# Kernel tuning notes

Hardware: AMD Instinct MI355X
Metric: run time of the kernel (lower is better)

Reference implementation:

```python
import jax, jax.numpy as jnp
import numpy as np

B, T, C, HS = 64, 256, 2048, 128


def setup_inputs() -> dict:
    key = jax.random.key(0)
    k1, k2, k3, k4 = jax.random.split(key, 4)
    x = jax.random.normal(k1, (B, T, C), dtype=jnp.float32)
    # Dense(head_size, use_bias=False) kernels, scaled like glorot-ish init
    Wk = jax.random.normal(k2, (C, HS), dtype=jnp.float32) * (C ** -0.5)
    Wq = jax.random.normal(k3, (C, HS), dtype=jnp.float32) * (C ** -0.5)
    Wv = jax.random.normal(k4, (C, HS), dtype=jnp.float32) * (C ** -0.5)
    return {"x": x, "Wk": Wk, "Wq": Wq, "Wv": Wv}


def reference(x, Wk, Wq, Wv):
    Bn, Tn, Cn = x.shape
    k = jnp.einsum("btc,ch->bth", x, Wk)
    q = jnp.einsum("btc,ch->bth", x, Wq)
    v = jnp.einsum("btc,ch->bth", x, Wv)
    # faithful to source: scores = k @ q^T, scaled by C**-0.5 (input dim!)
    scores = jnp.einsum("bth,bsh->bts", k, q) * (Cn ** -0.5)
    causal = jnp.tril(jnp.ones((Tn, Tn), dtype=bool))  # [T, T]
    scores = jnp.where(causal, scores, -jnp.inf)
    weights = jax.nn.softmax(scores, axis=-1)
    return jnp.einsum("bts,bsh->bth", weights, v)
```

## Files before the change

### kernel.cpp

```cpp
#include <hip/hip_runtime.h>
#include <hip/hip_bf16.h>
#include <cstdint>
#include <cstddef>

#define B_  64
#define T_  256
#define C_  2048
#define HS_ 128
#define N_  384

typedef __bf16 bf16x8 __attribute__((ext_vector_type(8)));
typedef float  floatx4 __attribute__((ext_vector_type(4)));

__device__ __forceinline__ unsigned short f2bf_rne(float f) {
  union { float f; unsigned int u; } v; v.f = f;
  unsigned int r = v.u + 0x7fffu + ((v.u >> 16) & 1u);
  return (unsigned short)(r >> 16);
}
__device__ __forceinline__ unsigned short f2bf(float f) {
  union { float f; unsigned int u; } v; v.f = f;
  return (unsigned short)((v.u + 0x8000u) >> 16);
}

__device__ __forceinline__ void async_copy16(const void* g, void* l) {
  __builtin_amdgcn_global_load_lds(
      (const __attribute__((address_space(1))) unsigned int*)g,
      (__attribute__((address_space(3))) unsigned int*)l, 16, 0, 0);
}

__global__ __launch_bounds__(256) void wt_kernel(
    const float* __restrict__ Wk, const float* __restrict__ Wq,
    const float* __restrict__ Wv, unsigned short* __restrict__ Wt) {
  __shared__ float tile[32][33];
  const int w  = blockIdx.z;
  const int c0 = blockIdx.x * 32;
  const int h0 = blockIdx.y * 32;
  const float* W = (w == 0) ? Wk : (w == 1) ? Wq : Wv;
  const int tx = threadIdx.x & 31, ty = threadIdx.x >> 5;
#pragma unroll
  for (int i = 0; i < 32; i += 8)
    tile[ty + i][tx] = W[(size_t)(c0 + ty + i) * HS_ + h0 + tx];
  __syncthreads();
#pragma unroll
  for (int i = 0; i < 32; i += 8) {
    int hh = ty + i, cc = tx;
    Wt[(size_t)(w * HS_ + h0 + hh) * C_ + c0 + cc] = f2bf_rne(tile[cc][hh]);
  }
}

__global__ __launch_bounds__(256) void qkv_gemm(
    const float* __restrict__ X, const unsigned short* __restrict__ Wt,
    unsigned short* __restrict__ kqv, unsigned short* __restrict__ vT) {
  __shared__ unsigned short As[64 * 72];
  __shared__ unsigned short Bs[128 * 64];

  const int tid  = threadIdx.x;
  const int wave = tid >> 6, lane = tid & 63;
  const int quad = lane >> 4, l16 = lane & 15;

  const int g  = blockIdx.x;
  const int ml = g & 7, q8 = g >> 3;
  const int nb = q8 % 3, mh = q8 / 3;
  const int m0 = (mh * 8 + ml) * 64;
  const int n0 = nb * 128;
  const int wm = (wave >> 1) * 32;
  const int wn = (wave & 1) * 64;

  const int arow = tid >> 4;
  const int achk = tid & 15;

  floatx4 acc[2][4] = {};

  for (int k0 = 0; k0 < C_; k0 += 64) {
#pragma unroll
    for (int r = 0; r < 4; ++r) {
      int slot = (r * 4 + wave) * 64 + lane;
      int n = slot >> 3, sl = slot & 7;
      int c = sl ^ (n & 7);
      async_copy16(Wt + (size_t)(n0 + n) * C_ + k0 + c * 8,
                   &Bs[(size_t)((r * 4 + wave) * 64) * 8]);
    }
    float4 av[4];
#pragma unroll
    for (int r = 0; r < 4; ++r)
      av[r] = *(const float4*)(X + (size_t)(m0 + arow + r * 16) * C_ + k0 + achk * 4);
#pragma unroll
    for (int r = 0; r < 4; ++r) {
      ushort4 b4;
      b4.x = f2bf(av[r].x); b4.y = f2bf(av[r].y);
      b4.z = f2bf(av[r].z); b4.w = f2bf(av[r].w);
      *(ushort4*)&As[(arow + r * 16) * 72 + achk * 4] = b4;
    }
    __syncthreads();

#pragma unroll
    for (int ks = 0; ks < 2; ++ks) {
      bf16x8 af[2], bfv[4];
#pragma unroll
      for (int mt = 0; mt < 2; ++mt)
        af[mt] = *(const bf16x8*)&As[(wm + mt * 16 + l16) * 72 + ks * 32 + quad * 8];
#pragma unroll
      for (int nt = 0; nt < 4; ++nt) {
        int n = wn + nt * 16 + l16;
        int c = ks * 4 + quad;
        bfv[nt] = *(const bf16x8*)&Bs[n * 64 + (c ^ (n & 7)) * 8];
      }
#pragma unroll
      for (int mt = 0; mt < 2; ++mt)
#pragma unroll
        for (int nt = 0; nt < 4; ++nt)
          acc[mt][nt] = __builtin_amdgcn_mfma_f32_16x16x32_bf16(
              af[mt], bfv[nt], acc[mt][nt], 0, 0, 0);
    }
    __syncthreads();
  }

#pragma unroll
  for (int mt = 0; mt < 2; ++mt)
#pragma unroll
    for (int nt = 0; nt < 4; ++nt)
#pragma unroll
      for (int r = 0; r < 4; ++r) {
        int row = m0 + wm + mt * 16 + quad * 4 + r;
        int col = wn + nt * 16 + l16;
        unsigned short us = f2bf(acc[mt][nt][r]);
        kqv[(size_t)row * N_ + n0 + col] = us;
        if (n0 == 256) {
          int bb = row >> 8, tt = row & 255;
          vT[(size_t)bb * HS_ * T_ + (size_t)col * T_ + tt] = us;
        }
      }
}

__global__ __launch_bounds__(64) void attn_kernel(
    const unsigned short* __restrict__ kqv, const unsigned short* __restrict__ vT,
    float* __restrict__ out) {
  __shared__ unsigned short P[16 * 264];
  const int lane = threadIdx.x;
  const int quad = lane >> 4, l16 = lane & 15;
  const int tb = blockIdx.x;
  const int b  = blockIdx.y;
  const int t0 = tb * 16;
  const float scale = 0.022097086912079612f;
  const unsigned short* kq = kqv + (size_t)b * T_ * N_;

  bf16x8 kf[4];
#pragma unroll
  for (int ks = 0; ks < 4; ++ks)
    kf[ks] = *(const bf16x8*)&kq[(size_t)(t0 + l16) * N_ + ks * 32 + quad * 8];

  floatx4 S[16];
#pragma unroll
  for (int st = 0; st < 16; ++st) {
    if (st <= tb) {
      floatx4 a = {};
#pragma unroll
      for (int ks = 0; ks < 4; ++ks) {
        bf16x8 qf = *(const bf16x8*)&kq[(size_t)(st * 16 + l16) * N_ + HS_ +
                                        ks * 32 + quad * 8];
        a = __builtin_amdgcn_mfma_f32_16x16x32_bf16(kf[ks], qf, a, 0, 0, 0);
      }
      S[st] = a;
    }
  }

  float rsum[4] = {0.f, 0.f, 0.f, 0.f};
#pragma unroll
  for (int st = 0; st < 16; ++st) {
    if (st <= tb) {
      int scol = st * 16 + l16;
#pragma unroll
      for (int r = 0; r < 4; ++r) {
        int trow = t0 + quad * 4 + r;
        float p = (scol <= trow) ? __expf(S[st][r] * scale) : 0.f;
        S[st][r] = p;
        rsum[r] += p;
      }
    }
  }
#pragma unroll
  for (int m = 1; m < 16; m <<= 1)
#pragma unroll
    for (int r = 0; r < 4; ++r)
      rsum[r] += __shfl_xor(rsum[r], m, 64);

  const int st_hi = (tb + 2) & ~1;
#pragma unroll
  for (int st = 0; st < 16; ++st) {
    if (st < st_hi) {
#pragma unroll
      for (int r = 0; r < 4; ++r) {
        float p = (st <= tb) ? S[st][r] : 0.f;
        P[(quad * 4 + r) * 264 + st * 16 + l16] = f2bf(p);
      }
    }
  }
  __syncthreads();

  floatx4 oacc[8] = {};
  const unsigned short* vb = vT + (size_t)b * HS_ * T_;
  const int nks = (tb + 2) >> 1;
#pragma unroll
  for (int ks = 0; ks < 8; ++ks) {
    if (ks < nks) {
      bf16x8 pa = *(const bf16x8*)&P[l16 * 264 + ks * 32 + quad * 8];
#pragma unroll
      for (int nt = 0; nt < 8; ++nt) {
        bf16x8 bv = *(const bf16x8*)&vb[(size_t)(nt * 16 + l16) * T_ +
                                        ks * 32 + quad * 8];
        oacc[nt] = __builtin_amdgcn_mfma_f32_16x16x32_bf16(pa, bv, oacc[nt], 0, 0, 0);
      }
    }
  }

  float* ob = out + ((size_t)b * T_ + t0) * HS_;
#pragma unroll
  for (int nt = 0; nt < 8; ++nt)
#pragma unroll
    for (int r = 0; r < 4; ++r) {
      int row = quad * 4 + r;
      ob[(size_t)row * HS_ + nt * 16 + l16] = oacc[nt][r] / rsum[r];
    }
}

extern "C" void kernel_launch(void* const* d_in, const int* in_sizes, int n_in,
                              void* d_out, int out_size, void* d_ws, size_t ws_size,
                              hipStream_t stream) {
  const float* x  = (const float*)d_in[0];
  const float* Wk = (const float*)d_in[1];
  const float* Wq = (const float*)d_in[2];
  const float* Wv = (const float*)d_in[3];
  float* out = (float*)d_out;

  char* ws = (char*)d_ws;
  unsigned short* Wt  = (unsigned short*)(ws);
  unsigned short* kqv = (unsigned short*)(ws + 1572864);
  unsigned short* vT  = (unsigned short*)(ws + 1572864 + 12582912);

  hipLaunchKernelGGL(wt_kernel, dim3(64, 4, 3), dim3(256), 0, stream, Wk, Wq, Wv, Wt);
  hipLaunchKernelGGL(qkv_gemm, dim3(768), dim3(256), 0, stream, x, Wt, kqv, vT);
  hipLaunchKernelGGL(attn_kernel, dim3(16, 64), dim3(64), 0, stream, kqv, vT, out);
}
```

Measured before the change: 254.0 us.

## Restructure QKV GEMM to register-streamed B and split attention across four waves

The QKV GEMM drops the LDS-staged weight tile. Each wave now streams its 48 weight columns straight from global memory into registers, prefetching one k-step ahead, while a double-buffered 64x32 tile of X is converted to bf16 and shared through LDS. The grid becomes 256x2 blocks with launch_bounds(256,2). The attention kernel uses four waves per block that split the score tiles round-robin and the output head dimension in quarters, with per-wave row sums combined through shared memory. The goal is more parallelism and less per-wave serial work, at the cost of the weights no longer being reused through LDS and a k-step of only 32 with a barrier on every iteration.

```diff
diff --git a/kernel.cpp b/kernel.cpp
--- a/kernel.cpp
+++ b/kernel.cpp
@@ -20,12 +20,6 @@
 __device__ __forceinline__ unsigned short f2bf(float f) {
   union { float f; unsigned int u; } v; v.f = f;
   return (unsigned short)((v.u + 0x8000u) >> 16);
-}
-
-__device__ __forceinline__ void async_copy16(const void* g, void* l) {
-  __builtin_amdgcn_global_load_lds(
-      (const __attribute__((address_space(1))) unsigned int*)g,
-      (__attribute__((address_space(3))) unsigned int*)l, 16, 0, 0);
 }
 
 __global__ __launch_bounds__(256) void wt_kernel(
@@ -48,99 +42,103 @@
   }
 }
 
-__global__ __launch_bounds__(256) void qkv_gemm(
+__global__ __launch_bounds__(256, 2) void qkv_gemm(
     const float* __restrict__ X, const unsigned short* __restrict__ Wt,
     unsigned short* __restrict__ kqv, unsigned short* __restrict__ vT) {
-  __shared__ unsigned short As[64 * 72];
-  __shared__ unsigned short Bs[128 * 64];
+  __shared__ unsigned short As[2][64 * 32];
 
   const int tid  = threadIdx.x;
   const int wave = tid >> 6, lane = tid & 63;
   const int quad = lane >> 4, l16 = lane & 15;
 
-  const int g  = blockIdx.x;
-  const int ml = g & 7, q8 = g >> 3;
-  const int nb = q8 % 3, mh = q8 / 3;
-  const int m0 = (mh * 8 + ml) * 64;
-  const int n0 = nb * 128;
-  const int wm = (wave >> 1) * 32;
-  const int wn = (wave & 1) * 64;
-
-  const int arow = tid >> 4;
-  const int achk = tid & 15;
-
-  floatx4 acc[2][4] = {};
-
-  for (int k0 = 0; k0 < C_; k0 += 64) {
-#pragma unroll
-    for (int r = 0; r < 4; ++r) {
-      int slot = (r * 4 + wave) * 64 + lane;
-      int n = slot >> 3, sl = slot & 7;
-      int c = sl ^ (n & 7);
-      async_copy16(Wt + (size_t)(n0 + n) * C_ + k0 + c * 8,
-                   &Bs[(size_t)((r * 4 + wave) * 64) * 8]);
-    }
-    float4 av[4];
-#pragma unroll
-    for (int r = 0; r < 4; ++r)
-      av[r] = *(const float4*)(X + (size_t)(m0 + arow + r * 16) * C_ + k0 + achk * 4);
-#pragma unroll
-    for (int r = 0; r < 4; ++r) {
-      ushort4 b4;
-      b4.x = f2bf(av[r].x); b4.y = f2bf(av[r].y);
-      b4.z = f2bf(av[r].z); b4.w = f2bf(av[r].w);
-      *(ushort4*)&As[(arow + r * 16) * 72 + achk * 4] = b4;
-    }
+  const int m0    = blockIdx.x * 64;
+  const int nbase = blockIdx.y * 192 + wave * 48;
+
+  const int arow  = tid >> 3;
+  const int acol4 = (tid & 7) * 4;
+
+  const float* Xr0 = X + (size_t)(m0 + arow) * C_ + acol4;
+  const float* Xr1 = X + (size_t)(m0 + arow + 32) * C_ + acol4;
+
+  const unsigned short* Bp[3];
+#pragma unroll
+  for (int nt = 0; nt < 3; ++nt)
+    Bp[nt] = Wt + (size_t)(nbase + nt * 16 + l16) * C_ + quad * 8;
+
+  float4 a0 = *(const float4*)(Xr0);
+  float4 a1 = *(const float4*)(Xr1);
+  bf16x8 bcur[3];
+#pragma unroll
+  for (int nt = 0; nt < 3; ++nt) bcur[nt] = *(const bf16x8*)(Bp[nt]);
+
+  floatx4 acc[4][3] = {};
+
+  for (int k = 0; k < 64; ++k) {
+    const int cur = k & 1;
+    ushort4 u0, u1;
+    u0.x = f2bf(a0.x); u0.y = f2bf(a0.y); u0.z = f2bf(a0.z); u0.w = f2bf(a0.w);
+    u1.x = f2bf(a1.x); u1.y = f2bf(a1.y); u1.z = f2bf(a1.z); u1.w = f2bf(a1.w);
+    *(ushort4*)&As[cur][arow * 32 + acol4]        = u0;
+    *(ushort4*)&As[cur][(arow + 32) * 32 + acol4] = u1;
     __syncthreads();
 
-#pragma unroll
-    for (int ks = 0; ks < 2; ++ks) {
-      bf16x8 af[2], bfv[4];
-#pragma unroll
-      for (int mt = 0; mt < 2; ++mt)
-        af[mt] = *(const bf16x8*)&As[(wm + mt * 16 + l16) * 72 + ks * 32 + quad * 8];
-#pragma unroll
-      for (int nt = 0; nt < 4; ++nt) {
-        int n = wn + nt * 16 + l16;
-        int c = ks * 4 + quad;
-        bfv[nt] = *(const bf16x8*)&Bs[n * 64 + (c ^ (n & 7)) * 8];
-      }
-#pragma unroll
-      for (int mt = 0; mt < 2; ++mt)
-#pragma unroll
-        for (int nt = 0; nt < 4; ++nt)
-          acc[mt][nt] = __builtin_amdgcn_mfma_f32_16x16x32_bf16(
-              af[mt], bfv[nt], acc[mt][nt], 0, 0, 0);
-    }
-    __syncthreads();
-  }
-
-#pragma unroll
-  for (int mt = 0; mt < 2; ++mt)
-#pragma unroll
-    for (int nt = 0; nt < 4; ++nt)
+    bf16x8 bnxt[3] = {bcur[0], bcur[1], bcur[2]};
+    if (k < 63) {
+      const int kn = (k + 1) * 32;
+      a0 = *(const float4*)(Xr0 + kn);
+      a1 = *(const float4*)(Xr1 + kn);
+#pragma unroll
+      for (int nt = 0; nt < 3; ++nt)
+        bnxt[nt] = *(const bf16x8*)(Bp[nt] + kn);
+    }
+
+    bf16x8 af[4];
+#pragma unroll
+    for (int mt = 0; mt < 4; ++mt)
+      af[mt] = *(const bf16x8*)&As[cur][(mt * 16 + l16) * 32 + quad * 8];
+#pragma unroll
+    for (int mt = 0; mt < 4; ++mt)
+#pragma unroll
+      for (int nt = 0; nt < 3; ++nt)
+        acc[mt][nt] = __builtin_amdgcn_mfma_f32_16x16x32_bf16(
+            af[mt], bcur[nt], acc[mt][nt], 0, 0, 0);
+#pragma unroll
+    for (int nt = 0; nt < 3; ++nt) bcur[nt] = bnxt[nt];
+  }
+
+#pragma unroll
+  for (int mt = 0; mt < 4; ++mt)
+#pragma unroll
+    for (int nt = 0; nt < 3; ++nt) {
+      const int n = nbase + nt * 16 + l16;
+      const bool isv = (nbase + nt * 16) >= 256;
 #pragma unroll
       for (int r = 0; r < 4; ++r) {
-        int row = m0 + wm + mt * 16 + quad * 4 + r;
-        int col = wn + nt * 16 + l16;
+        int m = m0 + mt * 16 + quad * 4 + r;
         unsigned short us = f2bf(acc[mt][nt][r]);
-        kqv[(size_t)row * N_ + n0 + col] = us;
-        if (n0 == 256) {
-          int bb = row >> 8, tt = row & 255;
-          vT[(size_t)bb * HS_ * T_ + (size_t)col * T_ + tt] = us;
+        kqv[(size_t)m * N_ + n] = us;
+        if (isv) {
+          int bb = m >> 8, tt = m & 255;
+          vT[(size_t)bb * HS_ * T_ + (size_t)(n - 256) * T_ + tt] = us;
         }
       }
-}
-
-__global__ __launch_bounds__(64) void attn_kernel(
+    }
+}
+
+__global__ __launch_bounds__(256) void attn_kernel(
     const unsigned short* __restrict__ kqv, const unsigned short* __restrict__ vT,
     float* __restrict__ out) {
-  __shared__ unsigned short P[16 * 264];
-  const int lane = threadIdx.x;
+  constexpr int PS = 264;
+  __shared__ unsigned short P[16 * PS];
+  __shared__ float rsumw[4][16];
+
+  const int tid  = threadIdx.x;
+  const int p    = tid >> 6;
+  const int lane = tid & 63;
   const int quad = lane >> 4, l16 = lane & 15;
-  const int tb = blockIdx.x;
+  const int tt = blockIdx.x;
   const int b  = blockIdx.y;
-  const int t0 = tb * 16;
+  const int t0 = tt * 16;
   const float scale = 0.022097086912079612f;
   const unsigned short* kq = kqv + (size_t)b * T_ * N_;
 
@@ -149,33 +147,28 @@
   for (int ks = 0; ks < 4; ++ks)
     kf[ks] = *(const bf16x8*)&kq[(size_t)(t0 + l16) * N_ + ks * 32 + quad * 8];
 
-  floatx4 S[16];
-#pragma unroll
-  for (int st = 0; st < 16; ++st) {
-    if (st <= tb) {
-      floatx4 a = {};
-#pragma unroll
-      for (int ks = 0; ks < 4; ++ks) {
-        bf16x8 qf = *(const bf16x8*)&kq[(size_t)(st * 16 + l16) * N_ + HS_ +
-                                        ks * 32 + quad * 8];
-        a = __builtin_amdgcn_mfma_f32_16x16x32_bf16(kf[ks], qf, a, 0, 0, 0);
-      }
-      S[st] = a;
-    }
+  if ((tt & 1) == 0 && p == ((tt + 1) & 3)) {
+#pragma unroll
+    for (int r = 0; r < 4; ++r)
+      P[(quad * 4 + r) * PS + (tt + 1) * 16 + l16] = 0;
   }
 
   float rsum[4] = {0.f, 0.f, 0.f, 0.f};
-#pragma unroll
-  for (int st = 0; st < 16; ++st) {
-    if (st <= tb) {
-      int scol = st * 16 + l16;
-#pragma unroll
-      for (int r = 0; r < 4; ++r) {
-        int trow = t0 + quad * 4 + r;
-        float p = (scol <= trow) ? __expf(S[st][r] * scale) : 0.f;
-        S[st][r] = p;
-        rsum[r] += p;
-      }
+  for (int st = p; st <= tt; st += 4) {
+    floatx4 a = {};
+#pragma unroll
+    for (int ks = 0; ks < 4; ++ks) {
+      bf16x8 qf = *(const bf16x8*)&kq[(size_t)(st * 16 + l16) * N_ + HS_ +
+                                      ks * 32 + quad * 8];
+      a = __builtin_amdgcn_mfma_f32_16x16x32_bf16(kf[ks], qf, a, 0, 0, 0);
+    }
+    const int scol = st * 16 + l16;
+#pragma unroll
+    for (int r = 0; r < 4; ++r) {
+      int trow = t0 + quad * 4 + r;
+      float pv = (scol <= trow) ? __expf(a[r] * scale) : 0.f;
+      rsum[r] += pv;
+      P[(quad * 4 + r) * PS + scol] = f2bf(pv);
     }
   }
 #pragma unroll
@@ -183,43 +176,39 @@
 #pragma unroll
     for (int r = 0; r < 4; ++r)
       rsum[r] += __shfl_xor(rsum[r], m, 64);
-
-  const int st_hi = (tb + 2) & ~1;
-#pragma unroll
-  for (int st = 0; st < 16; ++st) {
-    if (st < st_hi) {
-#pragma unroll
-      for (int r = 0; r < 4; ++r) {
-        float p = (st <= tb) ? S[st][r] : 0.f;
-        P[(quad * 4 + r) * 264 + st * 16 + l16] = f2bf(p);
-      }
-    }
+  if (l16 == 0) {
+#pragma unroll
+    for (int r = 0; r < 4; ++r) rsumw[p][quad * 4 + r] = rsum[r];
   }
   __syncthreads();
 
-  floatx4 oacc[8] = {};
   const unsigned short* vb = vT + (size_t)b * HS_ * T_;
-  const int nks = (tb + 2) >> 1;
-#pragma unroll
-  for (int ks = 0; ks < 8; ++ks) {
-    if (ks < nks) {
-      bf16x8 pa = *(const bf16x8*)&P[l16 * 264 + ks * 32 + quad * 8];
-#pragma unroll
-      for (int nt = 0; nt < 8; ++nt) {
-        bf16x8 bv = *(const bf16x8*)&vb[(size_t)(nt * 16 + l16) * T_ +
-                                        ks * 32 + quad * 8];
-        oacc[nt] = __builtin_amdgcn_mfma_f32_16x16x32_bf16(pa, bv, oacc[nt], 0, 0, 0);
-      }
-    }
-  }
-
+  const int h0 = p * 32;
+  const int nks = (tt + 2) >> 1;
+  floatx4 oacc[2] = {};
+  for (int ks = 0; ks < nks; ++ks) {
+    bf16x8 pa = *(const bf16x8*)&P[l16 * PS + ks * 32 + quad * 8];
+#pragma unroll
+    for (int nt = 0; nt < 2; ++nt) {
+      bf16x8 bv = *(const bf16x8*)&vb[(size_t)(h0 + nt * 16 + l16) * T_ +
+                                      ks * 32 + quad * 8];
+      oacc[nt] = __builtin_amdgcn_mfma_f32_16x16x32_bf16(pa, bv, oacc[nt], 0, 0, 0);
+    }
+  }
+
+  float tot[4];
+#pragma unroll
+  for (int r = 0; r < 4; ++r) {
+    int row = quad * 4 + r;
+    tot[r] = rsumw[0][row] + rsumw[1][row] + rsumw[2][row] + rsumw[3][row];
+  }
   float* ob = out + ((size_t)b * T_ + t0) * HS_;
 #pragma unroll
-  for (int nt = 0; nt < 8; ++nt)
+  for (int nt = 0; nt < 2; ++nt)
 #pragma unroll
     for (int r = 0; r < 4; ++r) {
       int row = quad * 4 + r;
-      ob[(size_t)row * HS_ + nt * 16 + l16] = oacc[nt][r] / rsum[r];
+      ob[(size_t)row * HS_ + h0 + nt * 16 + l16] = oacc[nt][r] / tot[r];
     }
 }
 
@@ -238,6 +227,6 @@
   unsigned short* vT  = (unsigned short*)(ws + 1572864 + 12582912);
 
   hipLaunchKernelGGL(wt_kernel, dim3(64, 4, 3), dim3(256), 0, stream, Wk, Wq, Wv, Wt);
-  hipLaunchKernelGGL(qkv_gemm, dim3(768), dim3(256), 0, stream, x, Wt, kqv, vT);
-  hipLaunchKernelGGL(attn_kernel, dim3(16, 64), dim3(64), 0, stream, kqv, vT, out);
-}
+  hipLaunchKernelGGL(qkv_gemm, dim3(256, 2), dim3(256), 0, stream, x, Wt, kqv, vT);
+  hipLaunchKernelGGL(attn_kernel, dim3(16, 64), dim3(256), 0, stream, kqv, vT, out);
+}
```

New measurement: 253.8 us. Within noise of the previous version (-0.1%).
